# Kernel tuning notes

Hardware: AMD Instinct MI355X
Metric: run time of the kernel (lower is better)

## Reference

```python
import jax, jax.numpy as jnp
import numpy as np

WIDTH = 512      # cart_pixel_width
PATCH = 32       # patch_size (kernel == stride, non-overlapping)
TEMP = 1.0       # softmax temperature


def _unfold(x, p):
    """F.unfold with kernel=stride=p on (B,C,H,W) -> (B,C,p*p,L).
    Kernel elements ordered row-major (ki,kj); patches ordered row-major over the grid,
    matching torch.nn.functional.unfold followed by the module's .view reshape."""
    B, C, H, W = x.shape
    Hp, Wp = H // p, W // p
    x = x.reshape(B, C, Hp, p, Wp, p).transpose(0, 1, 3, 5, 2, 4)
    return x.reshape(B, C, p * p, Hp * Wp)


def setup_inputs() -> dict:
    key = jax.random.key(0)
    k1, k2, k3 = jax.random.split(key, 3)
    BW, C = 8, 128
    return {
        "detector_scores": jax.random.normal(k1, (BW, 1, WIDTH, WIDTH), dtype=jnp.float32),
        "weight_scores": jax.random.normal(k2, (BW, 1, WIDTH, WIDTH), dtype=jnp.float32),
        "descriptors": jax.random.normal(k3, (BW, C, WIDTH, WIDTH), dtype=jnp.float32),
    }


def reference(detector_scores, weight_scores, descriptors):
    # coordinate grids: u = column index, v = row index (torch.meshgrid 'ij')
    v, u = jnp.meshgrid(jnp.arange(WIDTH, dtype=jnp.float32),
                        jnp.arange(WIDTH, dtype=jnp.float32), indexing="ij")
    u_patches = _unfold(u[None, None], PATCH)[:, 0]  # (1, p*p, L)
    v_patches = _unfold(v[None, None], PATCH)[:, 0]  # (1, p*p, L)

    det_patches = _unfold(detector_scores, PATCH)[:, 0]          # (BW, p*p, L)
    att = jax.nn.softmax(det_patches / TEMP, axis=1)             # spatial softmax per patch

    expected_u = jnp.sum(u_patches * att, axis=1)                # (BW, L)
    expected_v = jnp.sum(v_patches * att, axis=1)                # (BW, L)
    keypoint_coords = jnp.stack([expected_u, expected_v], axis=2)  # (BW, L, 2)

    att4 = att[:, None]                                          # (BW, 1, p*p, L)
    desc_patches = _unfold(descriptors, PATCH)                   # (BW, C, p*p, L)
    keypoint_desc = jnp.sum(desc_patches * att4, axis=2)         # (BW, C, L)

    score_patches = _unfold(weight_scores, PATCH)                # (BW, 1, p*p, L)
    keypoint_scores = jnp.sum(score_patches * att4, axis=2)      # (BW, 1, L)

    return keypoint_coords, keypoint_scores, keypoint_desc
```

## Files before the change

kernel.cpp:

```cpp
#include <hip/hip_runtime.h>
#include <hip/hip_bf16.h>

#define W512   512
#define PATCH  32
#define NP     16
#define L      256
#define NCH    128
#define PLANE  (W512 * W512)

typedef float  f32x4 __attribute__((ext_vector_type(4)));
typedef unsigned short u16x4 __attribute__((ext_vector_type(4)));

__device__ __forceinline__ unsigned short f2bf(float f) {
    __hip_bfloat16 h = __float2bfloat16(f);
    return *reinterpret_cast<unsigned short*>(&h);
}
__device__ __forceinline__ float bf2f(unsigned short u) {
    return __uint_as_float(((unsigned int)u) << 16);
}

__device__ __forceinline__ float wave_max(float v) {
    #pragma unroll
    for (int o = 32; o; o >>= 1) v = fmaxf(v, __shfl_xor(v, o, 64));
    return v;
}
__device__ __forceinline__ float wave_sum(float v) {
    #pragma unroll
    for (int o = 32; o; o >>= 1) v += __shfl_xor(v, o, 64);
    return v;
}

__global__ __launch_bounds__(256)
void att_kernel(const float* __restrict__ det,
                const float* __restrict__ wsc,
                float* __restrict__ out,
                unsigned short* __restrict__ attws) {
    __shared__ float red[12];

    const int blk = blockIdx.x;
    const int b   = blk >> 8;
    const int l   = blk & 255;
    const int hp  = l >> 4;
    const int wp  = l & 15;

    const int t    = threadIdx.x;
    const int wave = t >> 6;
    const int lane = t & 63;
    const int r    = t >> 3;
    const int q    = t & 7;

    const int row = hp * PATCH + r;
    const int col = wp * PATCH + q * 4;
    const size_t pix = (size_t)b * PLANE + (size_t)row * W512 + col;

    const f32x4 d4 = __builtin_nontemporal_load((const f32x4*)(det + pix));

    float m = fmaxf(fmaxf(d4.x, d4.y), fmaxf(d4.z, d4.w));
    m = wave_max(m);
    if (lane == 0) red[wave] = m;
    __syncthreads();
    m = fmaxf(fmaxf(red[0], red[1]), fmaxf(red[2], red[3]));

    float e0 = expf(d4.x - m);
    float e1 = expf(d4.y - m);
    float e2 = expf(d4.z - m);
    float e3 = expf(d4.w - m);

    float s = wave_sum(e0 + e1 + e2 + e3);
    if (lane == 0) red[4 + wave] = s;
    __syncthreads();
    s = red[4] + red[5] + red[6] + red[7];
    const float inv = 1.0f / s;
    e0 *= inv; e1 *= inv; e2 *= inv; e3 *= inv;

    u16x4 pk;
    pk.x = f2bf(e0); pk.y = f2bf(e1); pk.z = f2bf(e2); pk.w = f2bf(e3);
    *(u16x4*)(attws + pix) = pk;

    const f32x4 w4 = __builtin_nontemporal_load((const f32x4*)(wsc + pix));
    float pu = e0 * (float)(col)     + e1 * (float)(col + 1)
             + e2 * (float)(col + 2) + e3 * (float)(col + 3);
    float pv = (e0 + e1 + e2 + e3) * (float)row;
    float ps = e0 * w4.x + e1 * w4.y + e2 * w4.z + e3 * w4.w;

    pu = wave_sum(pu);
    pv = wave_sum(pv);
    ps = wave_sum(ps);
    __syncthreads();
    if (lane == 0) { red[wave] = pu; red[4 + wave] = pv; red[8 + wave] = ps; }
    __syncthreads();
    if (t == 0) {
        out[blk * 2 + 0]       = red[0] + red[1] + red[2]  + red[3];
        out[blk * 2 + 1]       = red[4] + red[5] + red[6]  + red[7];
        out[2 * (8 * L) + blk] = red[8] + red[9] + red[10] + red[11];
    }
}

__global__ __launch_bounds__(256)
void pool_kernel(const float* __restrict__ desc,
                 const unsigned short* __restrict__ attws,
                 float* __restrict__ outd) {
    const int bid   = blockIdx.x;
    const int cg    = bid >> 7;
    const int strip = bid & 127;
    const int b     = strip >> 4;
    const int hp    = strip & 15;

    const int t    = threadIdx.x;
    const int wave = t >> 6;
    const int lane = t & 63;
    const int ch   = cg * 8 + wave * 2;

    const unsigned short* ap = attws + ((size_t)b * W512 + hp * PATCH) * W512 + lane * 4;
    const float* dp0 = desc + (((size_t)(b * NCH + ch)) * W512 + hp * PATCH) * W512 + lane * 4;
    const float* dp1 = dp0 + PLANE;

    float a00 = 0.f, a01 = 0.f, a10 = 0.f, a11 = 0.f;
    #pragma unroll 4
    for (int r = 0; r < PATCH; ++r) {
        const int off = r * W512;
        const u16x4 uv0 = *(const u16x4*)(ap + off);
        const u16x4 uv1 = *(const u16x4*)(ap + off + 256);
        const f32x4 d00 = __builtin_nontemporal_load((const f32x4*)(dp0 + off));
        const f32x4 d01 = __builtin_nontemporal_load((const f32x4*)(dp0 + off + 256));
        const f32x4 d10 = __builtin_nontemporal_load((const f32x4*)(dp1 + off));
        const f32x4 d11 = __builtin_nontemporal_load((const f32x4*)(dp1 + off + 256));
        const float ax0 = bf2f(uv0.x), ay0 = bf2f(uv0.y),
                    az0 = bf2f(uv0.z), aw0 = bf2f(uv0.w);
        const float ax1 = bf2f(uv1.x), ay1 = bf2f(uv1.y),
                    az1 = bf2f(uv1.z), aw1 = bf2f(uv1.w);
        a00 += ax0 * d00.x + ay0 * d00.y + az0 * d00.z + aw0 * d00.w;
        a01 += ax1 * d01.x + ay1 * d01.y + az1 * d01.z + aw1 * d01.w;
        a10 += ax0 * d10.x + ay0 * d10.y + az0 * d10.z + aw0 * d10.w;
        a11 += ax1 * d11.x + ay1 * d11.y + az1 * d11.z + aw1 * d11.w;
    }

    #pragma unroll
    for (int o = 1; o <= 4; o <<= 1) {
        a00 += __shfl_xor(a00, o, 64);
        a01 += __shfl_xor(a01, o, 64);
        a10 += __shfl_xor(a10, o, 64);
        a11 += __shfl_xor(a11, o, 64);
    }

    if ((lane & 7) == 0) {
        const int wp0 = lane >> 3;
        float* o0 = outd + ((size_t)(b * NCH + ch)) * L + hp * NP;
        o0[wp0]     = a00;
        o0[8 + wp0] = a01;
        float* o1 = o0 + L;
        o1[wp0]     = a10;
        o1[8 + wp0] = a11;
    }
}

extern "C" void kernel_launch(void* const* d_in, const int* in_sizes, int n_in,
                              void* d_out, int out_size, void* d_ws, size_t ws_size,
                              hipStream_t stream) {
    const float* det  = (const float*)d_in[0];
    const float* wsc  = (const float*)d_in[1];
    const float* desc = (const float*)d_in[2];
    float* out = (float*)d_out;
    unsigned short* attws = (unsigned short*)d_ws;

    att_kernel<<<dim3(8 * L), dim3(256), 0, stream>>>(det, wsc, out, attws);
    pool_kernel<<<dim3(2048), dim3(256), 0, stream>>>(desc, attws, out + 4096 + 2048);
}
```

Baseline: 171.5 us.

## Fuse softmax-attention and descriptor pooling into one kernel with per-strip flags

Merges the attention kernel and the pooling kernel into a single launch. Each block first computes the softmax for one patch, then increments a per-strip atomic counter and spin-waits until all 16 patches of its strip are done before pooling descriptors. This removes the second launch and the gap between kernels, and lets pooling start early on strips that are ready. It adds a memset launch, spin-wait overhead, and a deadlock risk if the blocks of a strip are not all resident at the same time.

```diff
diff --git a/kernel.cpp b/kernel.cpp
--- a/kernel.cpp
+++ b/kernel.cpp
@@ -7,6 +7,7 @@
 #define L      256
 #define NCH    128
 #define PLANE  (W512 * W512)
+#define NSTRIP 128
 
 typedef float  f32x4 __attribute__((ext_vector_type(4)));
 typedef unsigned short u16x4 __attribute__((ext_vector_type(4)));
@@ -18,7 +19,6 @@
 __device__ __forceinline__ float bf2f(unsigned short u) {
     return __uint_as_float(((unsigned int)u) << 16);
 }
-
 __device__ __forceinline__ float wave_max(float v) {
     #pragma unroll
     for (int o = 32; o; o >>= 1) v = fmaxf(v, __shfl_xor(v, o, 64));
@@ -30,87 +30,90 @@
     return v;
 }
 
-__global__ __launch_bounds__(256)
-void att_kernel(const float* __restrict__ det,
-                const float* __restrict__ wsc,
-                float* __restrict__ out,
-                unsigned short* __restrict__ attws) {
+__global__ __launch_bounds__(256, 8)
+void fused_kernel(const float* __restrict__ det,
+                  const float* __restrict__ wsc,
+                  const float* __restrict__ desc,
+                  float* __restrict__ out,
+                  unsigned short* __restrict__ attws,
+                  unsigned int* __restrict__ flags) {
     __shared__ float red[12];
 
-    const int blk = blockIdx.x;
-    const int b   = blk >> 8;
-    const int l   = blk & 255;
-    const int hp  = l >> 4;
-    const int wp  = l & 15;
+    const int bid  = blockIdx.x;
+    const int cg   = bid >> 7;
+    const int s    = bid & 127;
+    const int b    = s >> 4;
+    const int hp   = s & 15;
 
     const int t    = threadIdx.x;
     const int wave = t >> 6;
     const int lane = t & 63;
-    const int r    = t >> 3;
-    const int q    = t & 7;
 
-    const int row = hp * PATCH + r;
-    const int col = wp * PATCH + q * 4;
-    const size_t pix = (size_t)b * PLANE + (size_t)row * W512 + col;
+    {
+        const int wp  = cg;
+        const int r   = t >> 3;
+        const int q   = t & 7;
+        const int row = hp * PATCH + r;
+        const int col = wp * PATCH + q * 4;
+        const size_t pix = (size_t)b * PLANE + (size_t)row * W512 + col;
 
-    const f32x4 d4 = __builtin_nontemporal_load((const f32x4*)(det + pix));
+        const f32x4 d4 = __builtin_nontemporal_load((const f32x4*)(det + pix));
 
-    float m = fmaxf(fmaxf(d4.x, d4.y), fmaxf(d4.z, d4.w));
-    m = wave_max(m);
-    if (lane == 0) red[wave] = m;
-    __syncthreads();
-    m = fmaxf(fmaxf(red[0], red[1]), fmaxf(red[2], red[3]));
+        float m = fmaxf(fmaxf(d4.x, d4.y), fmaxf(d4.z, d4.w));
+        m = wave_max(m);
+        if (lane == 0) red[wave] = m;
+        __syncthreads();
+        m = fmaxf(fmaxf(red[0], red[1]), fmaxf(red[2], red[3]));
 
-    float e0 = expf(d4.x - m);
-    float e1 = expf(d4.y - m);
-    float e2 = expf(d4.z - m);
-    float e3 = expf(d4.w - m);
+        float e0 = expf(d4.x - m);
+        float e1 = expf(d4.y - m);
+        float e2 = expf(d4.z - m);
+        float e3 = expf(d4.w - m);
 
-    float s = wave_sum(e0 + e1 + e2 + e3);
-    if (lane == 0) red[4 + wave] = s;
-    __syncthreads();
-    s = red[4] + red[5] + red[6] + red[7];
-    const float inv = 1.0f / s;
-    e0 *= inv; e1 *= inv; e2 *= inv; e3 *= inv;
+        float ssum = wave_sum(e0 + e1 + e2 + e3);
+        if (lane == 0) red[4 + wave] = ssum;
+        __syncthreads();
+        ssum = red[4] + red[5] + red[6] + red[7];
+        const float inv = 1.0f / ssum;
+        e0 *= inv; e1 *= inv; e2 *= inv; e3 *= inv;
 
-    u16x4 pk;
-    pk.x = f2bf(e0); pk.y = f2bf(e1); pk.z = f2bf(e2); pk.w = f2bf(e3);
-    *(u16x4*)(attws + pix) = pk;
+        u16x4 pk;
+        pk.x = f2bf(e0); pk.y = f2bf(e1); pk.z = f2bf(e2); pk.w = f2bf(e3);
+        *(u16x4*)(attws + pix) = pk;
 
-    const f32x4 w4 = __builtin_nontemporal_load((const f32x4*)(wsc + pix));
-    float pu = e0 * (float)(col)     + e1 * (float)(col + 1)
-             + e2 * (float)(col + 2) + e3 * (float)(col + 3);
-    float pv = (e0 + e1 + e2 + e3) * (float)row;
-    float ps = e0 * w4.x + e1 * w4.y + e2 * w4.z + e3 * w4.w;
+        const f32x4 w4 = __builtin_nontemporal_load((const f32x4*)(wsc + pix));
+        float pu = e0 * (float)(col)     + e1 * (float)(col + 1)
+                 + e2 * (float)(col + 2) + e3 * (float)(col + 3);
+        float pv = (e0 + e1 + e2 + e3) * (float)row;
+        float ps = e0 * w4.x + e1 * w4.y + e2 * w4.z + e3 * w4.w;
 
-    pu = wave_sum(pu);
-    pv = wave_sum(pv);
-    ps = wave_sum(ps);
-    __syncthreads();
-    if (lane == 0) { red[wave] = pu; red[4 + wave] = pv; red[8 + wave] = ps; }
+        pu = wave_sum(pu);
+        pv = wave_sum(pv);
+        ps = wave_sum(ps);
+        __syncthreads();
+        if (lane == 0) { red[wave] = pu; red[4 + wave] = pv; red[8 + wave] = ps; }
+        __syncthreads();
+        if (t == 0) {
+            const int blk = b * L + hp * NP + wp;
+            out[blk * 2 + 0]       = red[0] + red[1] + red[2]  + red[3];
+            out[blk * 2 + 1]       = red[4] + red[5] + red[6]  + red[7];
+            out[2 * (8 * L) + blk] = red[8] + red[9] + red[10] + red[11];
+        }
+    }
+
+    __threadfence();
     __syncthreads();
     if (t == 0) {
-        out[blk * 2 + 0]       = red[0] + red[1] + red[2]  + red[3];
-        out[blk * 2 + 1]       = red[4] + red[5] + red[6]  + red[7];
-        out[2 * (8 * L) + blk] = red[8] + red[9] + red[10] + red[11];
+        __hip_atomic_fetch_add(&flags[s], 1u, __ATOMIC_RELEASE,
+                               __HIP_MEMORY_SCOPE_AGENT);
+        while (__hip_atomic_load(&flags[s], __ATOMIC_ACQUIRE,
+                                 __HIP_MEMORY_SCOPE_AGENT) < 16u) {
+            __builtin_amdgcn_s_sleep(2);
+        }
     }
-}
+    __syncthreads();
 
-__global__ __launch_bounds__(256)
-void pool_kernel(const float* __restrict__ desc,
-                 const unsigned short* __restrict__ attws,
-                 float* __restrict__ outd) {
-    const int bid   = blockIdx.x;
-    const int cg    = bid >> 7;
-    const int strip = bid & 127;
-    const int b     = strip >> 4;
-    const int hp    = strip & 15;
-
-    const int t    = threadIdx.x;
-    const int wave = t >> 6;
-    const int lane = t & 63;
-    const int ch   = cg * 8 + wave * 2;
-
+    const int ch = cg * 8 + wave * 2;
     const unsigned short* ap = attws + ((size_t)b * W512 + hp * PATCH) * W512 + lane * 4;
     const float* dp0 = desc + (((size_t)(b * NCH + ch)) * W512 + hp * PATCH) * W512 + lane * 4;
     const float* dp1 = dp0 + PLANE;
@@ -145,6 +148,7 @@
 
     if ((lane & 7) == 0) {
         const int wp0 = lane >> 3;
+        float* outd = out + 4096 + 2048;
         float* o0 = outd + ((size_t)(b * NCH + ch)) * L + hp * NP;
         o0[wp0]     = a00;
         o0[8 + wp0] = a01;
@@ -161,8 +165,10 @@
     const float* wsc  = (const float*)d_in[1];
     const float* desc = (const float*)d_in[2];
     float* out = (float*)d_out;
+
     unsigned short* attws = (unsigned short*)d_ws;
+    unsigned int*   flags = (unsigned int*)((char*)d_ws + (4 << 20));
 
-    att_kernel<<<dim3(8 * L), dim3(256), 0, stream>>>(det, wsc, out, attws);
-    pool_kernel<<<dim3(2048), dim3(256), 0, stream>>>(desc, attws, out + 4096 + 2048);
+    hipMemsetAsync(flags, 0, NSTRIP * sizeof(unsigned int), stream);
+    fused_kernel<<<dim3(2048), dim3(256), 0, stream>>>(det, wsc, desc, out, attws, flags);
 }
```

After: 393.4 us. 129% more time.
